# Optimization experiments

Measured on AMD Instinct MI355X. Metric: run time of the kernel, lower is better.

The kernel has to match this reference:

```python
import jax, jax.numpy as jnp
import numpy as np

N = 3072        # nodes
NFEAT = 128
NHID = 64
NHEADS = 8
LENGTH = 8      # path length
NPATHS = 2048
NTASK = 4
ALPHA = 0.2     # LeakyReLU negative slope
NEG_INF = -9e15


def setup_inputs() -> dict:
    key = jax.random.key(0)
    ks = jax.random.split(key, 12)
    features = jax.random.normal(ks[0], (N, NFEAT), dtype=jnp.float32)
    adj = (jax.random.uniform(ks[1], (N, N)) < 0.01).astype(jnp.float32)
    adj = jnp.maximum(adj, jnp.eye(N, dtype=jnp.float32))
    path = jax.random.randint(ks[2], (NPATHS, LENGTH), 0, N)
    task = jax.random.randint(ks[3], (NPATHS * LENGTH,), 0, NTASK)
    s = 0.1
    Wp = jax.random.normal(ks[4], (NHEADS, NFEAT, NHID), dtype=jnp.float32) * s
    ap = jax.random.normal(ks[5], (NHEADS, 2 * NHID, 1), dtype=jnp.float32) * s
    Ws = jax.random.normal(ks[6], (NHEADS, NFEAT, NHID), dtype=jnp.float32) * s
    a_s = jax.random.normal(ks[7], (NHEADS, 2 * NHID, 1), dtype=jnp.float32) * s
    Wsc = jax.random.normal(ks[8], (NHID * NHEADS, NTASK), dtype=jnp.float32) * s
    bsc = jnp.zeros((NTASK,), dtype=jnp.float32)
    Wc = jax.random.normal(ks[9], (NHID * NHEADS * LENGTH * 2, 1), dtype=jnp.float32) * s
    bc = jnp.zeros((1,), dtype=jnp.float32)
    return dict(features=features, adj=adj, path=path, task=task,
                Wp=Wp, ap=ap, Ws=Ws, a_s=a_s, Wsc=Wsc, bsc=bsc, Wc=Wc, bc=bc)


def _gat_head(h, mask, W, a):
    # Dense GAT head: Wh [N,nhid]; e_ij = leakyrelu(a1.Wh_i + a2.Wh_j)
    Wh = h @ W                              # [N, nhid]
    f1 = Wh @ a[:NHID]                      # [N, 1]
    f2 = Wh @ a[NHID:]                      # [N, 1]
    e = jax.nn.leaky_relu(f1 + f2.T, negative_slope=ALPHA)  # [N, N]
    att = jax.nn.softmax(jnp.where(mask, e, NEG_INF), axis=1)
    return jax.nn.elu(att @ Wh)             # concat=True -> elu


def _multihead(h, mask, W, a):
    out = jax.vmap(_gat_head, in_axes=(None, None, 0, 0))(h, mask, W, a)  # [H,N,nhid]
    return jnp.transpose(out, (1, 0, 2)).reshape(h.shape[0], NHEADS * NHID)


def reference(features, adj, path, task, Wp, ap, Ws, a_s, Wsc, bsc, Wc, bc):
    mask = adj > 0
    private_x = _multihead(features, mask, Wp, ap)   # [N, H*nhid]
    share_x = _multihead(features, mask, Ws, a_s)    # [N, H*nhid]
    idx = path.reshape(-1)                           # [P*L]
    share_feature = share_x[idx]                     # [P*L, H*nhid]
    private_feature = private_x[idx]                 # [P*L, H*nhid]
    # adversarial task loss: cross_entropy(softmax(sigmoid(logits)), task)
    logits = share_feature @ Wsc + bsc
    node_task = jax.nn.softmax(jax.nn.sigmoid(logits), axis=1)
    logp = jax.nn.log_softmax(node_task, axis=1)
    adv_loss = -jnp.mean(jnp.take_along_axis(logp, task[:, None], axis=1))
    # diff loss: ||S^T P||_F^2
    diff = share_feature.T @ private_feature         # [H*nhid, H*nhid]
    diff_loss = jnp.sum(diff ** 2)
    x = jnp.concatenate([share_feature, private_feature], axis=1)
    x = x.reshape(-1, NHID * NHEADS * LENGTH * 2)    # [P, 8192]
    x = jax.nn.sigmoid(x @ Wc + bc)                  # [P, 1]
    return (x, adv_loss, diff_loss)
```

## Files before the change

kernel.cpp:

```cpp
#include <hip/hip_runtime.h>
#include <hip/hip_bf16.h>
#include <math.h>

#define NN     3072
#define NF     128
#define NHID   64
#define HEADS  8
#define LEN    8
#define NPATH  2048
#define NTK    4
#define NELEM  (NPATH*LEN)
#define MAXDEG 128
#define SH     16
#define KSPLIT 12
#define KCH    (NN / KSPLIT)
#define NADV   192
#define NDIF   256

__global__ void k_pre(const float* __restrict__ feat,
                      const float* __restrict__ Wp, const float* __restrict__ Ws,
                      const float* __restrict__ ap, const float* __restrict__ as_,
                      const float* __restrict__ adj,
                      float* __restrict__ whg, float* __restrict__ f1g,
                      float* __restrict__ f2g, int* __restrict__ cols,
                      int* __restrict__ cnt, int* __restrict__ hist,
                      int* __restrict__ histT, float* __restrict__ out) {
    __shared__ float Fs[32][68];
    __shared__ float Wsh[32][64];
    int b = blockIdx.x;
    int tid = threadIdx.x;
    if (b < 768) {
        int rt = b % 48, sh = b / 48;
        int set = sh >> 3, head = sh & 7;
        int g = sh >> 2, sg = sh & 3;
        const float* W = (set ? Ws : Wp) + (size_t)head * NF * NHID;
        const float* a = (set ? as_ : ap) + (size_t)head * 2 * NHID;
        int tc = (tid & 15) * 4;
        int tr = (tid >> 4) * 4;
        float acc[4][4] = {};
        for (int k0 = 0; k0 < NF; k0 += 32) {
            for (int i = tid; i < 512; i += 256) {
                int r = i >> 3, kq = (i & 7) * 4;
                float4 v = *(const float4*)&feat[(size_t)(rt * 64 + r) * NF + k0 + kq];
                Fs[kq + 0][r] = v.x; Fs[kq + 1][r] = v.y;
                Fs[kq + 2][r] = v.z; Fs[kq + 3][r] = v.w;
            }
            for (int i = tid; i < 512; i += 256) {
                int k = i >> 4, cq = (i & 15) * 4;
                *(float4*)&Wsh[k][cq] = *(const float4*)&W[(size_t)(k0 + k) * NHID + cq];
            }
            __syncthreads();
            #pragma unroll
            for (int k = 0; k < 32; ++k) {
                float4 av = *(const float4*)&Fs[k][tr];
                float4 bv = *(const float4*)&Wsh[k][tc];
                float a_[4] = {av.x, av.y, av.z, av.w};
                float b_[4] = {bv.x, bv.y, bv.z, bv.w};
                #pragma unroll
                for (int i = 0; i < 4; ++i)
                    #pragma unroll
                    for (int j = 0; j < 4; ++j) acc[i][j] += a_[i] * b_[j];
            }
            __syncthreads();
        }
        #pragma unroll
        for (int i = 0; i < 4; ++i)
            *(float4*)&whg[(((size_t)g * NN + rt * 64 + tr + i) * 4 + sg) * NHID + tc] =
                *(float4*)&acc[i][0];
        float4 a1 = *(const float4*)&a[tc];
        float4 a2 = *(const float4*)&a[NHID + tc];
        float p1[4], p2[4];
        #pragma unroll
        for (int i = 0; i < 4; ++i) {
            p1[i] = acc[i][0]*a1.x + acc[i][1]*a1.y + acc[i][2]*a1.z + acc[i][3]*a1.w;
            p2[i] = acc[i][0]*a2.x + acc[i][1]*a2.y + acc[i][2]*a2.z + acc[i][3]*a2.w;
        }
        #pragma unroll
        for (int o = 1; o < 16; o <<= 1) {
            #pragma unroll
            for (int i = 0; i < 4; ++i) {
                p1[i] += __shfl_xor(p1[i], o);
                p2[i] += __shfl_xor(p2[i], o);
            }
        }
        if ((tid & 15) == 0) {
            #pragma unroll
            for (int i = 0; i < 4; ++i) {
                f1g[((size_t)g * NN + rt * 64 + tr + i) * 4 + sg] = p1[i];
                f2g[((size_t)g * NN + rt * 64 + tr + i) * 4 + sg] = p2[i];
            }
        }
        return;
    }
    int cb = b - 768;
    if (cb < 64) {
        int i = cb * 256 + tid;
        if (i < NN) hist[i] = 0;
        if (i < NN * NTK) histT[i] = 0;
        if (i == 0) { out[NPATH] = 0.f; out[NPATH + 1] = 0.f; }
    }
    int row  = cb * 4 + (tid >> 6);
    int lane = tid & 63;
    const float* ar = adj + (size_t)row * NN;
    int* cr = cols + (size_t)row * MAXDEG;
    int base = 0;
    for (int c0 = 0; c0 < NN; c0 += 256) {
        float4 v = *(const float4*)&ar[c0 + lane * 4];
        float e[4] = {v.x, v.y, v.z, v.w};
        #pragma unroll
        for (int q = 0; q < 4; ++q) {
            bool pred = e[q] > 0.f;
            unsigned long long bb = __ballot(pred);
            int before = __popcll(bb & ((1ull << lane) - 1ull));
            if (pred && (base + before) < MAXDEG) cr[base + before] = c0 + lane * 4 + q;
            base += __popcll(bb);
        }
    }
    if (lane == 0) cnt[row] = base < MAXDEG ? base : MAXDEG;
}

__global__ void k_gat(const float* __restrict__ whg, const float* __restrict__ f1g,
                      const float* __restrict__ f2g, const int* __restrict__ cols,
                      const int* __restrict__ cnt, const int* __restrict__ path,
                      const int* __restrict__ task, int* __restrict__ hist,
                      int* __restrict__ histT, float* __restrict__ xo) {
    __shared__ float attT[4][MAXDEG][4];
    __shared__ int   cls[4][MAXDEG];
    int b = blockIdx.x;
    if (b < 64) {
        int i = b * 256 + threadIdx.x;
        int node = path[i];
        atomicAdd(&hist[node], 1);
        atomicAdd(&histT[node * NTK + task[i]], 1);
    }
    int g = (b & 7) >> 1;
    int node4 = ((b >> 3) << 1) | (b & 1);
    int w = threadIdx.x >> 6;
    int lane = threadIdx.x & 63;
    int node = node4 * 4 + w;
    int deg = cnt[node];
    const int* cl = cols + (size_t)node * MAXDEG;
    const float* f2p = f2g + (size_t)g * NN * 4;
    float4 f1q = *(const float4*)&f1g[((size_t)g * NN + node) * 4];
    float f1v[4] = {f1q.x, f1q.y, f1q.z, f1q.w};

    float e0[4], e1[4];
    #pragma unroll
    for (int t = 0; t < 2; ++t) {
        int l = lane + t * 64;
        bool valid = l < deg;
        int j = valid ? cl[l] : 0;
        if (valid) cls[w][l] = j;
        float4 q = *(const float4*)&f2p[(size_t)j * 4];
        float f2v[4] = {q.x, q.y, q.z, q.w};
        float* e = t ? e1 : e0;
        #pragma unroll
        for (int s = 0; s < 4; ++s) {
            float x = f1v[s] + f2v[s];
            x = (x >= 0.f) ? x : 0.2f * x;
            e[s] = valid ? x : -1e30f;
        }
    }
    float m[4], sl[4], inv[4];
    #pragma unroll
    for (int s = 0; s < 4; ++s) m[s] = fmaxf(e0[s], e1[s]);
    #pragma unroll
    for (int o = 32; o; o >>= 1)
        #pragma unroll
        for (int s = 0; s < 4; ++s) m[s] = fmaxf(m[s], __shfl_xor(m[s], o));
    float ex0[4], ex1[4];
    #pragma unroll
    for (int s = 0; s < 4; ++s) {
        ex0[s] = expf(e0[s] - m[s]);
        ex1[s] = expf(e1[s] - m[s]);
        sl[s] = ex0[s] + ex1[s];
    }
    #pragma unroll
    for (int o = 32; o; o >>= 1)
        #pragma unroll
        for (int s = 0; s < 4; ++s) sl[s] += __shfl_xor(sl[s], o);
    #pragma unroll
    for (int s = 0; s < 4; ++s) inv[s] = 1.f / sl[s];
    *(float4*)&attT[w][lane][0]      = make_float4(ex0[0], ex0[1], ex0[2], ex0[3]);
    *(float4*)&attT[w][lane + 64][0] = make_float4(ex1[0], ex1[1], ex1[2], ex1[3]);

    const float* base = whg + (size_t)g * NN * 256;
    float acc0 = 0.f, acc1 = 0.f, acc2 = 0.f, acc3 = 0.f;
    int l = 0;
    for (; l + 2 <= deg; l += 2) {
        int ja = cls[w][l], jb = cls[w][l + 1];
        const float* wa = base + (size_t)ja * 256 + lane;
        const float* wb = base + (size_t)jb * 256 + lane;
        float4 aa = *(const float4*)&attT[w][l][0];
        float4 ab = *(const float4*)&attT[w][l + 1][0];
        float va0 = wa[0], va1 = wa[64], va2 = wa[128], va3 = wa[192];
        float vb0 = wb[0], vb1 = wb[64], vb2 = wb[128], vb3 = wb[192];
        acc0 += aa.x * va0; acc1 += aa.y * va1; acc2 += aa.z * va2; acc3 += aa.w * va3;
        acc0 += ab.x * vb0; acc1 += ab.y * vb1; acc2 += ab.z * vb2; acc3 += ab.w * vb3;
    }
    if (l < deg) {
        int j = cls[w][l];
        const float* wr = base + (size_t)j * 256 + lane;
        float4 a4 = *(const float4*)&attT[w][l][0];
        acc0 += a4.x * wr[0];   acc1 += a4.y * wr[64];
        acc2 += a4.z * wr[128]; acc3 += a4.w * wr[192];
    }
    float accv[4] = {acc0, acc1, acc2, acc3};
    #pragma unroll
    for (int s = 0; s < 4; ++s) {
        float v = accv[s] * inv[s];
        v = (v > 0.f) ? v : (expf(v) - 1.f);
        int sh = g * 4 + s;
        int set = sh >> 3, head = sh & 7;
        xo[((size_t)set * NN + node) * (HEADS * NHID) + head * NHID + lane] = v;
    }
}

__global__ void k_diffadv(const float* __restrict__ S, const float* __restrict__ P,
                          const int* __restrict__ hist, const float* __restrict__ Wsc,
                          const float* __restrict__ bsc, const int* __restrict__ histT,
                          float* __restrict__ Dp, float* __restrict__ out) {
    __shared__ float As[64][68];
    __shared__ float Bs[64][68];
    int b = blockIdx.x;
    int tid = threadIdx.x;
    if (b >= 768) {
        int a_ = b - 768;
        int wave = tid >> 6;
        int lane = tid & 63;
        float sloc = 0.f;
        #pragma unroll
        for (int i = 0; i < 4; ++i) {
            int w = a_ * 16 + wave * 4 + i;
            const float* row = S + (size_t)w * (HEADS * NHID);
            float4 v0 = *(const float4*)&row[lane * 8];
            float4 v1 = *(const float4*)&row[lane * 8 + 4];
            float vv[8] = {v0.x, v0.y, v0.z, v0.w, v1.x, v1.y, v1.z, v1.w};
            float p[4] = {0.f, 0.f, 0.f, 0.f};
            #pragma unroll
            for (int qq = 0; qq < 8; ++qq) {
                float4 wv = *(const float4*)&Wsc[(lane * 8 + qq) * 4];
                p[0] += vv[qq] * wv.x; p[1] += vv[qq] * wv.y;
                p[2] += vv[qq] * wv.z; p[3] += vv[qq] * wv.w;
            }
            for (int o = 32; o; o >>= 1) {
                p[0] += __shfl_xor(p[0], o); p[1] += __shfl_xor(p[1], o);
                p[2] += __shfl_xor(p[2], o); p[3] += __shfl_xor(p[3], o);
            }
            if (lane == 0) {
                float sg[4], mx = -1e30f;
                for (int j = 0; j < 4; ++j) {
                    sg[j] = 1.f / (1.f + expf(-(p[j] + bsc[j])));
                    mx = fmaxf(mx, sg[j]);
                }
                float ex[4], se = 0.f;
                for (int j = 0; j < 4; ++j) { ex[j] = expf(sg[j] - mx); se += ex[j]; }
                float pr[4], pe = 0.f;
                for (int j = 0; j < 4; ++j) { pr[j] = ex[j] / se; }
                for (int j = 0; j < 4; ++j) { pe += expf(pr[j]); }
                float lse = logf(pe);
                for (int j = 0; j < 4; ++j)
                    sloc += (float)histT[w * NTK + j] * (pr[j] - lse);
            }
        }
        if (lane == 0) ((float*)As)[wave] = sloc;
        __syncthreads();
        if (tid == 0) {
            float t = ((float*)As)[0] + ((float*)As)[1] + ((float*)As)[2] + ((float*)As)[3];
            if (t != 0.f) atomicAdd(&out[NPATH], -t * (1.f / (float)NELEM));
        }
        return;
    }
    int z = b >> 6, rem = b & 63;
    int a0 = (rem >> 3) * 64, b0 = (rem & 7) * 64;
    int kbase = z * KCH;
    int tr = (tid >> 4) * 4, tc = (tid & 15) * 4;
    float acc[4][4] = {};
    for (int k0 = 0; k0 < KCH; k0 += 64) {
        for (int i = tid; i < 64 * 16; i += 256) {
            int k = i >> 4, c4 = (i & 15) * 4;
            int krow = kbase + k0 + k;
            float wgt = (float)hist[krow];
            float4 sv = *(const float4*)&S[(size_t)krow * 512 + a0 + c4];
            As[k][c4 + 0] = sv.x * wgt; As[k][c4 + 1] = sv.y * wgt;
            As[k][c4 + 2] = sv.z * wgt; As[k][c4 + 3] = sv.w * wgt;
            float4 pv = *(const float4*)&P[(size_t)krow * 512 + b0 + c4];
            Bs[k][c4 + 0] = pv.x; Bs[k][c4 + 1] = pv.y;
            Bs[k][c4 + 2] = pv.z; Bs[k][c4 + 3] = pv.w;
        }
        __syncthreads();
        #pragma unroll
        for (int k = 0; k < 64; ++k) {
            float4 av = *(const float4*)&As[k][tr];
            float4 bv = *(const float4*)&Bs[k][tc];
            float a_[4] = {av.x, av.y, av.z, av.w};
            float b_[4] = {bv.x, bv.y, bv.z, bv.w};
            #pragma unroll
            for (int i = 0; i < 4; ++i)
                #pragma unroll
                for (int j = 0; j < 4; ++j) acc[i][j] += a_[i] * b_[j];
        }
        __syncthreads();
    }
    float* dst = Dp + (size_t)z * 512 * 512;
    #pragma unroll
    for (int i = 0; i < 4; ++i)
        *(float4*)&dst[(size_t)(a0 + tr + i) * 512 + b0 + tc] = *(float4*)&acc[i][0];
}

__global__ void k_final(const float* __restrict__ S, const float* __restrict__ P,
                        const int* __restrict__ path, const float* __restrict__ Wc,
                        const float* __restrict__ bc, const float* __restrict__ Dp,
                        float* __restrict__ out) {
    __shared__ float red[256];
    int b = blockIdx.x;
    int tid = threadIdx.x;
    if (b >= NPATH) {
        int e4 = (b - NPATH) * 256 + tid;
        float4 a = {0.f, 0.f, 0.f, 0.f};
        for (int z = 0; z < KSPLIT; ++z) {
            float4 v = *(const float4*)&Dp[(size_t)z * 512 * 512 + (size_t)e4 * 4];
            a.x += v.x; a.y += v.y; a.z += v.z; a.w += v.w;
        }
        red[tid] = a.x * a.x + a.y * a.y + a.z * a.z + a.w * a.w;
        __syncthreads();
        for (int o = 128; o; o >>= 1) {
            if (tid < o) red[tid] += red[tid + o];
            __syncthreads();
        }
        if (tid == 0) atomicAdd(&out[NPATH + 1], red[0]);
        return;
    }
    float s = 0.f;
    for (int m4 = tid; m4 < 2048; m4 += 256) {
        int m = m4 * 4;
        int l = m >> 10, w = m & 1023;
        int node = path[b * LEN + l];
        float4 wv = *(const float4*)&Wc[m];
        const float* src = (w < 512) ? &S[(size_t)node * 512 + w]
                                     : &P[(size_t)node * 512 + (w - 512)];
        float4 xv = *(const float4*)src;
        s += xv.x * wv.x + xv.y * wv.y + xv.z * wv.z + xv.w * wv.w;
    }
    red[tid] = s;
    __syncthreads();
    for (int o = 128; o; o >>= 1) {
        if (tid < o) red[tid] += red[tid + o];
        __syncthreads();
    }
    if (tid == 0) out[b] = 1.f / (1.f + expf(-(red[0] + bc[0])));
}

extern "C" void kernel_launch(void* const* d_in, const int* in_sizes, int n_in,
                              void* d_out, int out_size, void* d_ws, size_t ws_size,
                              hipStream_t stream) {
    const float* feat = (const float*)d_in[0];
    const float* adj  = (const float*)d_in[1];
    const int*   path = (const int*)d_in[2];
    const int*   task = (const int*)d_in[3];
    const float* Wp   = (const float*)d_in[4];
    const float* ap   = (const float*)d_in[5];
    const float* Ws   = (const float*)d_in[6];
    const float* as_  = (const float*)d_in[7];
    const float* Wsc  = (const float*)d_in[8];
    const float* bsc  = (const float*)d_in[9];
    const float* Wc   = (const float*)d_in[10];
    const float* bc   = (const float*)d_in[11];
    float* out = (float*)d_out;

    float* whg   = (float*)d_ws;
    float* f1g   = whg + (size_t)NN * SH * NHID;
    float* f2g   = f1g + (size_t)NN * SH;
    float* xo    = f2g + (size_t)NN * SH;
    float* Dp    = xo + (size_t)2 * NN * 512;
    int*   cols  = (int*)(Dp + (size_t)KSPLIT * 512 * 512);
    int*   cnt   = cols + (size_t)NN * MAXDEG;
    int*   hist  = cnt + NN;
    int*   histT = hist + NN;

    float* Pm = xo;
    float* Sm = xo + (size_t)NN * 512;

    k_pre<<<1536, 256, 0, stream>>>(feat, Wp, Ws, ap, as_, adj,
                                    whg, f1g, f2g, cols, cnt, hist, histT, out);
    k_gat<<<NN, 256, 0, stream>>>(whg, f1g, f2g, cols, cnt, path, task, hist, histT, xo);
    k_diffadv<<<768 + NADV, 256, 0, stream>>>(Sm, Pm, hist, Wsc, bsc, histT, Dp, out);
    k_final<<<NPATH + NDIF, 256, 0, stream>>>(Sm, Pm, path, Wc, bc, Dp, out);
}
```

Baseline: 91.13 us.

## Precompute per-node classifier dots per path position instead of per-path gathers

Rather than gathering 8192 features per path and dotting them with Wc, the code precomputes an 8-element dot product for every node (one value per path position) and stores it in a new workspace buffer. The final kernel then only sums eight scalars per path. This replaces 2048 block-wide reductions over gathered rows with 3072 node passes that read each row once, and the classifier tail shrinks to a few blocks. It also lowers the diff-GEMM K-split from 12 to 8, giving fewer partials to reduce but fewer blocks.

```diff
diff --git a/kernel.cpp b/kernel.cpp
--- a/kernel.cpp
+++ b/kernel.cpp
@@ -12,9 +12,11 @@
 #define NELEM  (NPATH*LEN)
 #define MAXDEG 128
 #define SH     16
-#define KSPLIT 12
+#define KSPLIT 8
 #define KCH    (NN / KSPLIT)
+#define NDIFB  (KSPLIT * 64)
 #define NADV   192
+#define NNOD   48
 #define NDIF   256
 
 __global__ void k_pre(const float* __restrict__ feat,
@@ -219,13 +221,53 @@
 __global__ void k_diffadv(const float* __restrict__ S, const float* __restrict__ P,
                           const int* __restrict__ hist, const float* __restrict__ Wsc,
                           const float* __restrict__ bsc, const int* __restrict__ histT,
-                          float* __restrict__ Dp, float* __restrict__ out) {
-    __shared__ float As[64][68];
-    __shared__ float Bs[64][68];
+                          const float* __restrict__ Wc, float* __restrict__ Dp,
+                          float* __restrict__ nodeDot, float* __restrict__ out) {
+    __shared__ float4 shbuf[2176];
+    float* As = (float*)shbuf;
+    float* Bs = As + 64 * 68;
     int b = blockIdx.x;
     int tid = threadIdx.x;
-    if (b >= 768) {
-        int a_ = b - 768;
+    if (b < NDIFB) {
+        int z = b >> 6, rem = b & 63;
+        int a0 = (rem >> 3) * 64, b0 = (rem & 7) * 64;
+        int kbase = z * KCH;
+        int tr = (tid >> 4) * 4, tc = (tid & 15) * 4;
+        float acc[4][4] = {};
+        for (int k0 = 0; k0 < KCH; k0 += 64) {
+            for (int i = tid; i < 64 * 16; i += 256) {
+                int k = i >> 4, c4 = (i & 15) * 4;
+                int krow = kbase + k0 + k;
+                float wgt = (float)hist[krow];
+                float4 sv = *(const float4*)&S[(size_t)krow * 512 + a0 + c4];
+                As[k * 68 + c4 + 0] = sv.x * wgt; As[k * 68 + c4 + 1] = sv.y * wgt;
+                As[k * 68 + c4 + 2] = sv.z * wgt; As[k * 68 + c4 + 3] = sv.w * wgt;
+                float4 pv = *(const float4*)&P[(size_t)krow * 512 + b0 + c4];
+                Bs[k * 68 + c4 + 0] = pv.x; Bs[k * 68 + c4 + 1] = pv.y;
+                Bs[k * 68 + c4 + 2] = pv.z; Bs[k * 68 + c4 + 3] = pv.w;
+            }
+            __syncthreads();
+            #pragma unroll
+            for (int k = 0; k < 64; ++k) {
+                float4 av = *(const float4*)&As[k * 68 + tr];
+                float4 bv = *(const float4*)&Bs[k * 68 + tc];
+                float a_[4] = {av.x, av.y, av.z, av.w};
+                float b_[4] = {bv.x, bv.y, bv.z, bv.w};
+                #pragma unroll
+                for (int i = 0; i < 4; ++i)
+                    #pragma unroll
+                    for (int j = 0; j < 4; ++j) acc[i][j] += a_[i] * b_[j];
+            }
+            __syncthreads();
+        }
+        float* dst = Dp + (size_t)z * 512 * 512;
+        #pragma unroll
+        for (int i = 0; i < 4; ++i)
+            *(float4*)&dst[(size_t)(a0 + tr + i) * 512 + b0 + tc] = *(float4*)&acc[i][0];
+        return;
+    }
+    if (b < NDIFB + NADV) {
+        int a_ = b - NDIFB;
         int wave = tid >> 6;
         int lane = tid & 63;
         float sloc = 0.f;
@@ -263,92 +305,81 @@
                     sloc += (float)histT[w * NTK + j] * (pr[j] - lse);
             }
         }
-        if (lane == 0) ((float*)As)[wave] = sloc;
+        if (lane == 0) As[wave] = sloc;
         __syncthreads();
         if (tid == 0) {
-            float t = ((float*)As)[0] + ((float*)As)[1] + ((float*)As)[2] + ((float*)As)[3];
+            float t = As[0] + As[1] + As[2] + As[3];
             if (t != 0.f) atomicAdd(&out[NPATH], -t * (1.f / (float)NELEM));
         }
         return;
     }
-    int z = b >> 6, rem = b & 63;
-    int a0 = (rem >> 3) * 64, b0 = (rem & 7) * 64;
-    int kbase = z * KCH;
-    int tr = (tid >> 4) * 4, tc = (tid & 15) * 4;
-    float acc[4][4] = {};
-    for (int k0 = 0; k0 < KCH; k0 += 64) {
-        for (int i = tid; i < 64 * 16; i += 256) {
-            int k = i >> 4, c4 = (i & 15) * 4;
-            int krow = kbase + k0 + k;
-            float wgt = (float)hist[krow];
-            float4 sv = *(const float4*)&S[(size_t)krow * 512 + a0 + c4];
-            As[k][c4 + 0] = sv.x * wgt; As[k][c4 + 1] = sv.y * wgt;
-            As[k][c4 + 2] = sv.z * wgt; As[k][c4 + 3] = sv.w * wgt;
-            float4 pv = *(const float4*)&P[(size_t)krow * 512 + b0 + c4];
-            Bs[k][c4 + 0] = pv.x; Bs[k][c4 + 1] = pv.y;
-            Bs[k][c4 + 2] = pv.z; Bs[k][c4 + 3] = pv.w;
-        }
-        __syncthreads();
-        #pragma unroll
-        for (int k = 0; k < 64; ++k) {
-            float4 av = *(const float4*)&As[k][tr];
-            float4 bv = *(const float4*)&Bs[k][tc];
-            float a_[4] = {av.x, av.y, av.z, av.w};
-            float b_[4] = {bv.x, bv.y, bv.z, bv.w};
-            #pragma unroll
-            for (int i = 0; i < 4; ++i)
-                #pragma unroll
-                for (int j = 0; j < 4; ++j) acc[i][j] += a_[i] * b_[j];
-        }
-        __syncthreads();
-    }
-    float* dst = Dp + (size_t)z * 512 * 512;
-    #pragma unroll
-    for (int i = 0; i < 4; ++i)
-        *(float4*)&dst[(size_t)(a0 + tr + i) * 512 + b0 + tc] = *(float4*)&acc[i][0];
+    int nb = b - NDIFB - NADV;
+    float4* WcL = shbuf;
+    for (int i = tid; i < 2048; i += 256) WcL[i] = ((const float4*)Wc)[i];
+    __syncthreads();
+    int wave = tid >> 6;
+    int lane = tid & 63;
+    const float4* Sf4 = (const float4*)S;
+    const float4* Pf4 = (const float4*)P;
+    for (int t = 0; t < 16; ++t) {
+        int n = nb * 64 + wave * 16 + t;
+        float4 v0 = Sf4[(size_t)n * 128 + lane];
+        float4 v1 = Sf4[(size_t)n * 128 + 64 + lane];
+        float4 v2 = Pf4[(size_t)n * 128 + lane];
+        float4 v3 = Pf4[(size_t)n * 128 + 64 + lane];
+        float d[8];
+        #pragma unroll
+        for (int l = 0; l < 8; ++l) {
+            float4 w0 = WcL[l * 256 + lane];
+            float4 w1 = WcL[l * 256 + 64 + lane];
+            float4 w2 = WcL[l * 256 + 128 + lane];
+            float4 w3 = WcL[l * 256 + 192 + lane];
+            d[l] = v0.x*w0.x + v0.y*w0.y + v0.z*w0.z + v0.w*w0.w
+                 + v1.x*w1.x + v1.y*w1.y + v1.z*w1.z + v1.w*w1.w
+                 + v2.x*w2.x + v2.y*w2.y + v2.z*w2.z + v2.w*w2.w
+                 + v3.x*w3.x + v3.y*w3.y + v3.z*w3.z + v3.w*w3.w;
+        }
+        #pragma unroll
+        for (int o = 32; o; o >>= 1)
+            #pragma unroll
+            for (int l = 0; l < 8; ++l) d[l] += __shfl_xor(d[l], o);
+        if (lane == 0) {
+            *(float4*)&nodeDot[(size_t)n * 8]     = make_float4(d[0], d[1], d[2], d[3]);
+            *(float4*)&nodeDot[(size_t)n * 8 + 4] = make_float4(d[4], d[5], d[6], d[7]);
+        }
+    }
 }
 
-__global__ void k_final(const float* __restrict__ S, const float* __restrict__ P,
-                        const int* __restrict__ path, const float* __restrict__ Wc,
+__global__ void k_final(const int* __restrict__ path, const float* __restrict__ nodeDot,
                         const float* __restrict__ bc, const float* __restrict__ Dp,
                         float* __restrict__ out) {
     __shared__ float red[256];
     int b = blockIdx.x;
     int tid = threadIdx.x;
-    if (b >= NPATH) {
-        int e4 = (b - NPATH) * 256 + tid;
-        float4 a = {0.f, 0.f, 0.f, 0.f};
-        for (int z = 0; z < KSPLIT; ++z) {
-            float4 v = *(const float4*)&Dp[(size_t)z * 512 * 512 + (size_t)e4 * 4];
-            a.x += v.x; a.y += v.y; a.z += v.z; a.w += v.w;
-        }
-        red[tid] = a.x * a.x + a.y * a.y + a.z * a.z + a.w * a.w;
-        __syncthreads();
-        for (int o = 128; o; o >>= 1) {
-            if (tid < o) red[tid] += red[tid + o];
-            __syncthreads();
-        }
-        if (tid == 0) atomicAdd(&out[NPATH + 1], red[0]);
+    if (b < 8) {
+        int p = b * 256 + tid;
+        float s = bc[0];
+        #pragma unroll
+        for (int l = 0; l < 8; ++l) {
+            int node = path[p * LEN + l];
+            s += nodeDot[(size_t)node * 8 + l];
+        }
+        out[p] = 1.f / (1.f + expf(-s));
         return;
     }
-    float s = 0.f;
-    for (int m4 = tid; m4 < 2048; m4 += 256) {
-        int m = m4 * 4;
-        int l = m >> 10, w = m & 1023;
-        int node = path[b * LEN + l];
-        float4 wv = *(const float4*)&Wc[m];
-        const float* src = (w < 512) ? &S[(size_t)node * 512 + w]
-                                     : &P[(size_t)node * 512 + (w - 512)];
-        float4 xv = *(const float4*)src;
-        s += xv.x * wv.x + xv.y * wv.y + xv.z * wv.z + xv.w * wv.w;
-    }
-    red[tid] = s;
+    int e4 = (b - 8) * 256 + tid;
+    float4 a = {0.f, 0.f, 0.f, 0.f};
+    for (int z = 0; z < KSPLIT; ++z) {
+        float4 v = *(const float4*)&Dp[(size_t)z * 512 * 512 + (size_t)e4 * 4];
+        a.x += v.x; a.y += v.y; a.z += v.z; a.w += v.w;
+    }
+    red[tid] = a.x * a.x + a.y * a.y + a.z * a.z + a.w * a.w;
     __syncthreads();
     for (int o = 128; o; o >>= 1) {
         if (tid < o) red[tid] += red[tid + o];
         __syncthreads();
     }
-    if (tid == 0) out[b] = 1.f / (1.f + expf(-(red[0] + bc[0])));
+    if (tid == 0) atomicAdd(&out[NPATH + 1], red[0]);
 }
 
 extern "C" void kernel_launch(void* const* d_in, const int* in_sizes, int n_in,
@@ -368,15 +399,16 @@
     const float* bc   = (const float*)d_in[11];
     float* out = (float*)d_out;
 
-    float* whg   = (float*)d_ws;
-    float* f1g   = whg + (size_t)NN * SH * NHID;
-    float* f2g   = f1g + (size_t)NN * SH;
-    float* xo    = f2g + (size_t)NN * SH;
-    float* Dp    = xo + (size_t)2 * NN * 512;
-    int*   cols  = (int*)(Dp + (size_t)KSPLIT * 512 * 512);
-    int*   cnt   = cols + (size_t)NN * MAXDEG;
-    int*   hist  = cnt + NN;
-    int*   histT = hist + NN;
+    float* whg    = (float*)d_ws;
+    float* f1g    = whg + (size_t)NN * SH * NHID;
+    float* f2g    = f1g + (size_t)NN * SH;
+    float* xo     = f2g + (size_t)NN * SH;
+    float* Dp     = xo + (size_t)2 * NN * 512;
+    float* nodeDot= Dp + (size_t)KSPLIT * 512 * 512;
+    int*   cols   = (int*)(nodeDot + (size_t)NN * 8);
+    int*   cnt    = cols + (size_t)NN * MAXDEG;
+    int*   hist   = cnt + NN;
+    int*   histT  = hist + NN;
 
     float* Pm = xo;
     float* Sm = xo + (size_t)NN * 512;
@@ -384,6 +416,7 @@
     k_pre<<<1536, 256, 0, stream>>>(feat, Wp, Ws, ap, as_, adj,
                                     whg, f1g, f2g, cols, cnt, hist, histT, out);
     k_gat<<<NN, 256, 0, stream>>>(whg, f1g, f2g, cols, cnt, path, task, hist, histT, xo);
-    k_diffadv<<<768 + NADV, 256, 0, stream>>>(Sm, Pm, hist, Wsc, bsc, histT, Dp, out);
-    k_final<<<NPATH + NDIF, 256, 0, stream>>>(Sm, Pm, path, Wc, bc, Dp, out);
+    k_diffadv<<<NDIFB + NADV + NNOD, 256, 0, stream>>>(Sm, Pm, hist, Wsc, bsc, histT,
+                                                       Wc, Dp, nodeDot, out);
+    k_final<<<8 + NDIF, 256, 0, stream>>>(path, nodeDot, bc, Dp, out);
 }
```

Result: slower. 124.1 us (+36.2%).
